# Performance work log

Measured on AMD Instinct MI355X. Metric: run time of the kernel, lower is better.

## Reference

```python
import jax, jax.numpy as jnp
import numpy as np

D_MODEL = 512
STATE_DIM = 6
D_STATE = 16
D_CONV = 4
EXPAND = 2
D_INNER = EXPAND * D_MODEL            # 1024
DT_RANK = -(-D_MODEL // 16)           # ceil(d_model/16) = 32


def setup_inputs() -> dict:
    key = jax.random.key(0)
    ks = jax.random.split(key, 12)
    s = 0.02
    return {
        "features": jax.random.normal(ks[0], (32, 2048, D_MODEL), dtype=jnp.float32),
        # Mamba params (mamba_ssm defaults: in/out_proj bias=False, conv+dt_proj bias=True)
        "in_proj_w": jax.random.normal(ks[1], (2 * D_INNER, D_MODEL), dtype=jnp.float32) * s,
        "conv_w": jax.random.normal(ks[2], (D_INNER, D_CONV), dtype=jnp.float32) * s,
        "conv_b": jnp.zeros((D_INNER,), dtype=jnp.float32),
        "x_proj_w": jax.random.normal(ks[3], (DT_RANK + 2 * D_STATE, D_INNER), dtype=jnp.float32) * s,
        "dt_proj_w": jax.random.normal(ks[4], (D_INNER, DT_RANK), dtype=jnp.float32) * s,
        "dt_proj_b": jax.random.normal(ks[5], (D_INNER,), dtype=jnp.float32) * s,
        "A_log": jnp.log(jnp.broadcast_to(jnp.arange(1, D_STATE + 1, dtype=jnp.float32), (D_INNER, D_STATE))),
        "D": jnp.ones((D_INNER,), dtype=jnp.float32),
        "out_proj_w": jax.random.normal(ks[6], (D_MODEL, D_INNER), dtype=jnp.float32) * s,
        # trailing fc head: d_model -> state_dim**2
        "fc_w": jax.random.normal(ks[7], (STATE_DIM * STATE_DIM, D_MODEL), dtype=jnp.float32) * s,
        "fc_b": jnp.zeros((STATE_DIM * STATE_DIM,), dtype=jnp.float32),
    }


def reference(features, in_proj_w, conv_w, conv_b, x_proj_w, dt_proj_w, dt_proj_b,
              A_log, D, out_proj_w, fc_w, fc_b):
    # Original loops Mamba over timesteps with seq_len=1 slices -> each timestep is
    # independent. Flatten (batch, seq) into one token axis and vectorize.
    B_, T, dm = features.shape
    f = features.reshape(B_ * T, dm)                      # (N, d_model)

    xz = f @ in_proj_w.T                                  # (N, 2*d_inner)
    x, z = jnp.split(xz, 2, axis=-1)
    # causal depthwise conv on a length-1 sequence: only the last tap contributes
    x = jax.nn.silu(x * conv_w[:, -1] + conv_b)           # (N, d_inner)

    x_dbl = x @ x_proj_w.T                                # (N, dt_rank + 2*d_state)
    dt = x_dbl[:, :DT_RANK]
    Bm = x_dbl[:, DT_RANK:DT_RANK + D_STATE]              # (N, d_state)
    Cm = x_dbl[:, DT_RANK + D_STATE:]                     # (N, d_state)
    delta = jax.nn.softplus(dt @ dt_proj_w.T + dt_proj_b) # (N, d_inner)

    # single-step selective scan with h0 = 0:
    #   h = exp(delta*A)*0 + delta*B*x ;  y = sum_s C_s h_s + D*x
    # (A_log therefore never affects the output for seq_len=1 calls)
    bc = jnp.sum(Bm * Cm, axis=-1, keepdims=True)         # (N, 1)
    y = delta * x * bc + D * x                            # (N, d_inner)
    y = y * jax.nn.silu(z)

    out = y @ out_proj_w.T                                # (N, d_model)
    A_flat = out @ fc_w.T + fc_b                          # (N, state_dim**2)
    return A_flat.reshape(B_, T, STATE_DIM, STATE_DIM)
```

## Files before the change

kernel.cpp:

```cpp
#include <hip/hip_runtime.h>

typedef unsigned short u16;
typedef unsigned int u32;
typedef __attribute__((ext_vector_type(8))) short bf16x8;
typedef __attribute__((ext_vector_type(4))) float f32x4;

#define NTOK 65536
#define DM 512
#define DI 1024

__device__ __forceinline__ float bf2f(u16 u){ u32 x=((u32)u)<<16; float f; __builtin_memcpy(&f,&x,4); return f; }
__device__ __forceinline__ u16 f2bf(float f){ u32 u; __builtin_memcpy(&u,&f,4); u += 0x7fffu + ((u>>16)&1u); return (u16)(u>>16); }
__device__ __forceinline__ float siluf(float x){ return x/(1.f+__expf(-x)); }
__device__ __forceinline__ float softplus_fast(float x){
  float l = __logf(1.f + __expf(x));
  return (x > 20.f) ? x : l;
}

__device__ __forceinline__ void gload_lds16(const void* g, void* l){
  __builtin_amdgcn_global_load_lds((const __attribute__((address_space(1))) u32*)g,
                                   (__attribute__((address_space(3))) u32*)l, 16, 0, 0);
}

__global__ void k_sentinel(float* out){ out[0] = 1.2345e6f; }

__global__ void k_cast_bf16(const float* __restrict__ in, u16* __restrict__ out, int n){
  int i = (blockIdx.x*256 + threadIdx.x)*4;
  if (i >= n) return;
  float4 v = *(const float4*)(in + i);
  ushort4 o; o.x=f2bf(v.x); o.y=f2bf(v.y); o.z=f2bf(v.z); o.w=f2bf(v.w);
  *(ushort4*)(out + i) = o;
}

__global__ void k_make_wa(const float* __restrict__ fcw, const float* __restrict__ opw,
                          u16* __restrict__ wa){
  int j = blockIdx.x*256 + threadIdx.x;
  int i = blockIdx.y;
  float s = 0.f;
  if (i < 36){
    const float* fr = fcw + i*DM;
    #pragma unroll 8
    for (int k=0;k<DM;++k) s += fr[k]*opw[(size_t)k*DI + j];
  }
  wa[(size_t)i*DI + j] = f2bf(s);
}

__global__ __launch_bounds__(256) void k_gemm_xz(
  const u16* __restrict__ A, const u16* __restrict__ B,
  const float* __restrict__ convw, const float* __restrict__ convb,
  u16* __restrict__ xp, u16* __restrict__ zs)
{
  __shared__ u16 smem[32768];
  u16* SA = smem;
  u16* SB = smem + 16384;
  const int tid=threadIdx.x, wv=tid>>6, ln=tid&63;
  const int l15=ln&15, l4=ln>>4, h=l15&7;
  const int c0g=blockIdx.x*128, r0=blockIdx.y*128;
  const int wm=wv>>1, wn=wv&1;
  const int sr=ln>>3, scs=((ln&7)^sr)*8;
  const int chk0=(l4^h)*8, chk1=((l4+4)^h)*8;
  const int rA=(wm*64+l15)*64, rB=(wn*64+l15)*64;
  f32x4 acc[4][4]={};

  auto STAGE=[&](int buf, int k0){
    u16* Ad = SA + buf*8192;
    u16* Bd = SB + buf*8192;
    #pragma unroll
    for (int it=0;it<4;++it){
      int c=wv*4+it;
      gload_lds16(A + (size_t)(r0 + c*8 + sr)*DM + k0 + scs, Ad + c*512);
    }
    #pragma unroll
    for (int it=0;it<4;++it){
      int c=wv*4+it;
      gload_lds16(B + (size_t)(c0g + c*8 + sr)*DM + k0 + scs, Bd + c*512);
    }
  };

  STAGE(0, 0);
  __syncthreads();
  __builtin_amdgcn_sched_barrier(0);
  int cur = 0;
  #pragma clang loop unroll(disable)
  for (int t=0;t<8;++t){
    if (t < 7) STAGE(cur^1, (t+1)*64);
    const u16* Ac = SA + cur*8192;
    const u16* Bc = SB + cur*8192;
    #pragma unroll
    for (int kk=0;kk<2;++kk){
      const int ch = kk ? chk1 : chk0;
      bf16x8 af[4], bfr[4];
      #pragma unroll
      for (int m=0;m<4;++m) af[m]=*(const bf16x8*)(Ac + rA + m*1024 + ch);
      #pragma unroll
      for (int n=0;n<4;++n) bfr[n]=*(const bf16x8*)(Bc + rB + n*1024 + ch);
      #pragma unroll
      for (int m=0;m<4;++m)
        #pragma unroll
        for (int n=0;n<4;++n)
          acc[m][n]=__builtin_amdgcn_mfma_f32_16x16x32_bf16(af[m],bfr[n],acc[m][n],0,0,0);
    }
    __syncthreads();
    __builtin_amdgcn_sched_barrier(0);
    cur ^= 1;
  }

  const bool isx = (c0g < DI);
  const int cc0 = isx ? c0g : c0g - DI;
  u16* ep = smem;
  #pragma unroll
  for (int n=0;n<4;++n){
    int tcol = wn*64 + n*16 + l15;
    int gcol = c0g + tcol;
    float cw = isx ? convw[gcol*4+3] : 0.f;
    float cb = isx ? convb[gcol]     : 0.f;
    #pragma unroll
    for (int m=0;m<4;++m){
      int trow = wm*64 + m*16 + l4*4;
      #pragma unroll
      for (int r=0;r<4;++r){
        float v = acc[m][n][r];
        float o = isx ? siluf(v*cw + cb) : siluf(v);
        ep[(trow+r)*160 + tcol] = f2bf(o);
      }
    }
  }
  __syncthreads();
  int rrow = tid>>1, half = tid&1;
  const u16* srcp = ep + rrow*160 + half*64;
  u16* dst = (isx ? xp : zs) + (size_t)(r0+rrow)*DI + cc0 + half*64;
  #pragma unroll
  for (int j=0;j<8;++j)
    *(int4*)(dst + j*8) = *(const int4*)(srcp + j*8);
}

__global__ void k_bcdt(const float* __restrict__ xd, u16* __restrict__ dtb, float* __restrict__ bc){
  int t = blockIdx.x*256 + threadIdx.x;
  if (t >= NTOK) return;
  const float4* p = (const float4*)(xd + (size_t)t*64);
  #pragma unroll
  for (int q=0;q<8;++q){
    float4 v = p[q];
    ushort4 o; o.x=f2bf(v.x); o.y=f2bf(v.y); o.z=f2bf(v.z); o.w=f2bf(v.w);
    *(ushort4*)(dtb + (size_t)t*32 + q*4) = o;
  }
  float s=0.f;
  #pragma unroll
  for (int q=0;q<4;++q){
    float4 b = p[8+q], c = p[12+q];
    s += b.x*c.x + b.y*c.y + b.z*c.z + b.w*c.w;
  }
  bc[t]=s;
}

template<int EPI>
__global__ __launch_bounds__(256) void k_gemm_n64(
  const u16* __restrict__ A, const u16* __restrict__ B,
  float* __restrict__ xd, const float* __restrict__ fcb, float* __restrict__ out)
{
  __shared__ u16 smem[24576];
  u16* SA = smem;
  u16* SB = smem + 16384;
  const int tid=threadIdx.x, wv=tid>>6, ln=tid&63;
  const int l15=ln&15, l4=ln>>4, h=l15&7;
  const int r0=blockIdx.x*128;
  const int wm=wv>>1, wn=wv&1;
  const int sr=ln>>3, scs=((ln&7)^sr)*8;
  const int chk0=(l4^h)*8, chk1=((l4+4)^h)*8;
  const int rA=(wm*64+l15)*64, rB=(wn*32+l15)*64;
  f32x4 acc[4][2]={};

  auto STAGE=[&](int buf, int k0){
    u16* Ad = SA + buf*8192;
    u16* Bd = SB + buf*4096;
    #pragma unroll
    for (int it=0;it<4;++it){
      int c=wv*4+it;
      gload_lds16(A + (size_t)(r0 + c*8 + sr)*DI + k0 + scs, Ad + c*512);
    }
    #pragma unroll
    for (int it=0;it<2;++it){
      int c=wv*2+it;
      gload_lds16(B + (size_t)(c*8 + sr)*DI + k0 + scs, Bd + c*512);
    }
  };

  STAGE(0, 0);
  __syncthreads();
  __builtin_amdgcn_sched_barrier(0);
  int cur = 0;
  #pragma clang loop unroll(disable)
  for (int t=0;t<16;++t){
    if (t < 15) STAGE(cur^1, (t+1)*64);
    const u16* Ac = SA + cur*8192;
    const u16* Bc = SB + cur*4096;
    #pragma unroll
    for (int kk=0;kk<2;++kk){
      const int ch = kk ? chk1 : chk0;
      bf16x8 af[4], bfr[2];
      #pragma unroll
      for (int m=0;m<4;++m) af[m]=*(const bf16x8*)(Ac + rA + m*1024 + ch);
      #pragma unroll
      for (int n=0;n<2;++n) bfr[n]=*(const bf16x8*)(Bc + rB + n*1024 + ch);
      #pragma unroll
      for (int m=0;m<4;++m)
        #pragma unroll
        for (int n=0;n<2;++n)
          acc[m][n]=__builtin_amdgcn_mfma_f32_16x16x32_bf16(af[m],bfr[n],acc[m][n],0,0,0);
    }
    __syncthreads();
    __builtin_amdgcn_sched_barrier(0);
    cur ^= 1;
  }
  #pragma unroll
  for (int n=0;n<2;++n){
    int j = wn*32 + n*16 + l15;
    #pragma unroll
    for (int m=0;m<4;++m){
      #pragma unroll
      for (int r=0;r<4;++r){
        int t = r0 + wm*64 + m*16 + l4*4 + r;
        float v = acc[m][n][r];
        if (EPI==0) xd[(size_t)t*64 + j] = v;
        else if (j < 36) out[(size_t)t*36 + j] = v + fcb[j];
      }
    }
  }
}

__global__ __launch_bounds__(256) void k_delta_y(
  const u16* __restrict__ dtb, const u16* __restrict__ Bw,
  const float* __restrict__ dpb, const float* __restrict__ Dv,
  const float* __restrict__ bc,
  const u16* __restrict__ xp, u16* __restrict__ zy)
{
  __shared__ u16 smem[17408];
  u16* As = smem;
  u16* Bs = smem + 4096;
  const int tid=threadIdx.x, wv=tid>>6, ln=tid&63;
  const int l15=ln&15, l4=ln>>4;
  const int c0=blockIdx.x*128, r0=blockIdx.y*128;
  const int wm=wv>>1, wn=wv&1;
  const int sr=ln>>2, sc=(ln&3)*8;
  #pragma unroll
  for (int it=0;it<2;++it){
    int c=wv*2+it;
    gload_lds16(dtb + (size_t)(r0 + c*16 + sr)*32 + sc, As + c*512);
  }
  #pragma unroll
  for (int it=0;it<2;++it){
    int c=wv*2+it;
    gload_lds16(Bw + (size_t)(c0 + c*16 + sr)*32 + sc, Bs + c*512);
  }
  __syncthreads();
  __builtin_amdgcn_sched_barrier(0);
  f32x4 acc[4][4]={};
  bf16x8 af[4], bfr[4];
  #pragma unroll
  for (int m=0;m<4;++m) af[m]=*(const bf16x8*)(As + (wm*64+m*16+l15)*32 + l4*8);
  #pragma unroll
  for (int n=0;n<4;++n) bfr[n]=*(const bf16x8*)(Bs + (wn*64+n*16+l15)*32 + l4*8);
  #pragma unroll
  for (int m=0;m<4;++m)
    #pragma unroll
    for (int n=0;n<4;++n)
      acc[m][n]=__builtin_amdgcn_mfma_f32_16x16x32_bf16(af[m],bfr[n],acc[m][n],0,0,0);
  __syncthreads();
  u16* W = smem;
  #pragma unroll
  for (int n=0;n<4;++n){
    int tcol = wn*64 + n*16 + l15;
    int j = c0 + tcol;
    float dpbj = dpb[j], Dj = Dv[j];
    #pragma unroll
    for (int m=0;m<4;++m){
      int trow = wm*64 + m*16 + l4*4;
      #pragma unroll
      for (int r=0;r<4;++r){
        float delta = softplus_fast(acc[m][n][r] + dpbj);
        float w = delta*bc[r0 + trow + r] + Dj;
        W[(trow+r)*136 + tcol] = f2bf(w);
      }
    }
  }
  __syncthreads();
  const int row = tid>>1, half = tid&1;
  const u16* wp = W + row*136 + half*64;
  const size_t gbase = (size_t)(r0 + row)*DI + c0 + half*64;
  const u16* xpp = xp + gbase;
  u16* zp = zy + gbase;
  #pragma unroll
  for (int q=0;q<8;++q){
    bf16x8 wv8 = *(const bf16x8*)(wp + q*8);
    bf16x8 xv  = *(const bf16x8*)(xpp + q*8);
    bf16x8 zv  = *(const bf16x8*)(zp + q*8);
    bf16x8 ov;
    #pragma unroll
    for (int e=0;e<8;++e){
      float y = bf2f((u16)wv8[e]) * bf2f((u16)xv[e]) * bf2f((u16)zv[e]);
      ov[e] = (short)f2bf(y);
    }
    *(bf16x8*)(zp + q*8) = ov;
  }
}

extern "C" void kernel_launch(void* const* d_in, const int* in_sizes, int n_in,
                              void* d_out, int out_size, void* d_ws, size_t ws_size,
                              hipStream_t stream){
  const float* f      = (const float*)d_in[0];
  const float* inpw   = (const float*)d_in[1];
  const float* convw  = (const float*)d_in[2];
  const float* convb  = (const float*)d_in[3];
  const float* xprojw = (const float*)d_in[4];
  const float* dtpw   = (const float*)d_in[5];
  const float* dtpb   = (const float*)d_in[6];
  const float* Dv     = (const float*)d_in[8];
  const float* opw    = (const float*)d_in[9];
  const float* fcw    = (const float*)d_in[10];
  const float* fcb    = (const float*)d_in[11];
  float* out = (float*)d_out;

  char* ws = (char*)d_ws;
  size_t off = 0;
  auto alloc = [&](size_t sz)->void*{ void* p = ws + off; off += (sz + 255) & ~(size_t)255; return p; };
  u16*   fbf = (u16*)  alloc((size_t)NTOK*DM*2);
  u16*   xp  = (u16*)  alloc((size_t)NTOK*DI*2);
  u16*   zy  = (u16*)  alloc((size_t)NTOK*DI*2);
  float* xd  = (float*)alloc((size_t)NTOK*64*4);
  u16*   dtb = (u16*)  alloc((size_t)NTOK*32*2);
  float* bc  = (float*)alloc((size_t)NTOK*4);
  u16*   ipw = (u16*)  alloc((size_t)2048*512*2);
  u16*   xpw = (u16*)  alloc((size_t)64*1024*2);
  u16*   dpw = (u16*)  alloc((size_t)1024*32*2);
  u16*   wa  = (u16*)  alloc((size_t)64*1024*2);
  if (off > ws_size){ k_sentinel<<<1,1,0,stream>>>(out); return; }

  k_cast_bf16<<<dim3((NTOK*DM/4)/256),256,0,stream>>>(f, fbf, NTOK*DM);
  k_cast_bf16<<<dim3((2048*512/4)/256),256,0,stream>>>(inpw, ipw, 2048*512);
  k_cast_bf16<<<dim3((64*1024/4)/256),256,0,stream>>>(xprojw, xpw, 64*1024);
  k_cast_bf16<<<dim3((1024*32/4)/256),256,0,stream>>>(dtpw, dpw, 1024*32);
  k_make_wa<<<dim3(4,64),256,0,stream>>>(fcw, opw, wa);

  k_gemm_xz<<<dim3(16,512),256,0,stream>>>(fbf, ipw, convw, convb, xp, zy);
  k_gemm_n64<0><<<dim3(512),256,0,stream>>>(xp, xpw, xd, nullptr, nullptr);
  k_bcdt<<<dim3(NTOK/256),256,0,stream>>>(xd, dtb, bc);
  k_delta_y<<<dim3(8,512),256,0,stream>>>(dtb, dpw, dtpb, Dv, bc, xp, zy);
  k_gemm_n64<1><<<dim3(512),256,0,stream>>>(zy, wa, nullptr, fcb, out);
}
```

Measured before the change: 539.3 us.

## Triple-buffer xz GEMM with 8 waves, XCD-aware tile order, fuse bcdt into x_proj epilogue

The in_proj GEMM now runs 512-thread blocks, with each wave computing a 32x64 sub-tile. It uses a three-stage LDS ring with explicit vmcnt waits and a single barrier per k-step, and remaps the 1D grid so that blocks sharing a row tile land on the same XCD for L2 reuse. The k_bcdt kernel and its fp32 xd intermediate are removed. The x_proj GEMM epilogue now writes bf16 dt and the B·C dot product directly through LDS. This cuts one launch and a 16MB round trip, at the cost of larger LDS use and lower occupancy in the main GEMM.

```diff
diff --git a/kernel.cpp b/kernel.cpp
--- a/kernel.cpp
+++ b/kernel.cpp
@@ -45,65 +45,67 @@
   wa[(size_t)i*DI + j] = f2bf(s);
 }
 
-__global__ __launch_bounds__(256) void k_gemm_xz(
+__global__ __launch_bounds__(512) void k_gemm_xz(
   const u16* __restrict__ A, const u16* __restrict__ B,
   const float* __restrict__ convw, const float* __restrict__ convb,
   u16* __restrict__ xp, u16* __restrict__ zs)
 {
-  __shared__ u16 smem[32768];
-  u16* SA = smem;
-  u16* SB = smem + 16384;
+  __shared__ u16 smem[49152];
   const int tid=threadIdx.x, wv=tid>>6, ln=tid&63;
   const int l15=ln&15, l4=ln>>4, h=l15&7;
-  const int c0g=blockIdx.x*128, r0=blockIdx.y*128;
+  const int d = blockIdx.x;
+  const int xcd = d & 7, q = d >> 3;
+  const int g = xcd + 8*(q >> 4);
+  const int mcb = q & 15;
+  const int r0 = g*128, c0g = mcb*128;
   const int wm=wv>>1, wn=wv&1;
   const int sr=ln>>3, scs=((ln&7)^sr)*8;
   const int chk0=(l4^h)*8, chk1=((l4+4)^h)*8;
-  const int rA=(wm*64+l15)*64, rB=(wn*64+l15)*64;
-  f32x4 acc[4][4]={};
-
-  auto STAGE=[&](int buf, int k0){
-    u16* Ad = SA + buf*8192;
-    u16* Bd = SB + buf*8192;
-    #pragma unroll
-    for (int it=0;it<4;++it){
-      int c=wv*4+it;
+  f32x4 acc[2][4]={};
+
+  auto STAGE=[&](int buf, int kt){
+    const int k0 = kt*64;
+    u16* Ad = smem + buf*16384;
+    u16* Bd = Ad + 8192;
+    #pragma unroll
+    for (int it=0;it<2;++it){
+      int c=wv*2+it;
       gload_lds16(A + (size_t)(r0 + c*8 + sr)*DM + k0 + scs, Ad + c*512);
     }
     #pragma unroll
-    for (int it=0;it<4;++it){
-      int c=wv*4+it;
+    for (int it=0;it<2;++it){
+      int c=wv*2+it;
       gload_lds16(B + (size_t)(c0g + c*8 + sr)*DM + k0 + scs, Bd + c*512);
     }
   };
 
-  STAGE(0, 0);
-  __syncthreads();
-  __builtin_amdgcn_sched_barrier(0);
-  int cur = 0;
+  STAGE(0,0); STAGE(1,1);
   #pragma clang loop unroll(disable)
   for (int t=0;t<8;++t){
-    if (t < 7) STAGE(cur^1, (t+1)*64);
-    const u16* Ac = SA + cur*8192;
-    const u16* Bc = SB + cur*8192;
+    if (t<7) asm volatile("s_waitcnt vmcnt(4)" ::: "memory");
+    else     asm volatile("s_waitcnt vmcnt(0)" ::: "memory");
+    __builtin_amdgcn_s_barrier();
+    __builtin_amdgcn_sched_barrier(0);
+    if (t+2<8) STAGE((t+2)%3, t+2);
+    const u16* Ac = smem + (t%3)*16384;
+    const u16* Bc = Ac + 8192;
     #pragma unroll
     for (int kk=0;kk<2;++kk){
       const int ch = kk ? chk1 : chk0;
-      bf16x8 af[4], bfr[4];
-      #pragma unroll
-      for (int m=0;m<4;++m) af[m]=*(const bf16x8*)(Ac + rA + m*1024 + ch);
-      #pragma unroll
-      for (int n=0;n<4;++n) bfr[n]=*(const bf16x8*)(Bc + rB + n*1024 + ch);
-      #pragma unroll
-      for (int m=0;m<4;++m)
+      bf16x8 af[2], bfr[4];
+      #pragma unroll
+      for (int m=0;m<2;++m) af[m]=*(const bf16x8*)(Ac + (wm*32+m*16+l15)*64 + ch);
+      #pragma unroll
+      for (int n=0;n<4;++n) bfr[n]=*(const bf16x8*)(Bc + (wn*64+n*16+l15)*64 + ch);
+      #pragma unroll
+      for (int m=0;m<2;++m)
         #pragma unroll
         for (int n=0;n<4;++n)
           acc[m][n]=__builtin_amdgcn_mfma_f32_16x16x32_bf16(af[m],bfr[n],acc[m][n],0,0,0);
     }
-    __syncthreads();
     __builtin_amdgcn_sched_barrier(0);
-    cur ^= 1;
-  }
+  }
+  __syncthreads();
 
   const bool isx = (c0g < DI);
   const int cc0 = isx ? c0g : c0g - DI;
@@ -115,8 +117,8 @@
     float cw = isx ? convw[gcol*4+3] : 0.f;
     float cb = isx ? convb[gcol]     : 0.f;
     #pragma unroll
-    for (int m=0;m<4;++m){
-      int trow = wm*64 + m*16 + l4*4;
+    for (int m=0;m<2;++m){
+      int trow = wm*32 + m*16 + l4*4;
       #pragma unroll
       for (int r=0;r<4;++r){
         float v = acc[m][n][r];
@@ -126,37 +128,19 @@
     }
   }
   __syncthreads();
-  int rrow = tid>>1, half = tid&1;
-  const u16* srcp = ep + rrow*160 + half*64;
-  u16* dst = (isx ? xp : zs) + (size_t)(r0+rrow)*DI + cc0 + half*64;
-  #pragma unroll
-  for (int j=0;j<8;++j)
-    *(int4*)(dst + j*8) = *(const int4*)(srcp + j*8);
-}
-
-__global__ void k_bcdt(const float* __restrict__ xd, u16* __restrict__ dtb, float* __restrict__ bc){
-  int t = blockIdx.x*256 + threadIdx.x;
-  if (t >= NTOK) return;
-  const float4* p = (const float4*)(xd + (size_t)t*64);
-  #pragma unroll
-  for (int q=0;q<8;++q){
-    float4 v = p[q];
-    ushort4 o; o.x=f2bf(v.x); o.y=f2bf(v.y); o.z=f2bf(v.z); o.w=f2bf(v.w);
-    *(ushort4*)(dtb + (size_t)t*32 + q*4) = o;
-  }
-  float s=0.f;
-  #pragma unroll
-  for (int q=0;q<4;++q){
-    float4 b = p[8+q], c = p[12+q];
-    s += b.x*c.x + b.y*c.y + b.z*c.z + b.w*c.w;
-  }
-  bc[t]=s;
+  const int rrow = tid>>2, qq = tid&3;
+  const u16* srcp = ep + rrow*160 + qq*32;
+  u16* dst = (isx ? xp : zs) + (size_t)(r0+rrow)*DI + cc0 + qq*32;
+  #pragma unroll
+  for (int j=0;j<4;++j)
+    ((int4*)dst)[j] = ((const int4*)srcp)[j];
 }
 
 template<int EPI>
 __global__ __launch_bounds__(256) void k_gemm_n64(
   const u16* __restrict__ A, const u16* __restrict__ B,
-  float* __restrict__ xd, const float* __restrict__ fcb, float* __restrict__ out)
+  u16* __restrict__ dtb, float* __restrict__ bc,
+  const float* __restrict__ fcb, float* __restrict__ out)
 {
   __shared__ u16 smem[24576];
   u16* SA = smem;
@@ -212,17 +196,49 @@
     __builtin_amdgcn_sched_barrier(0);
     cur ^= 1;
   }
-  #pragma unroll
-  for (int n=0;n<2;++n){
-    int j = wn*32 + n*16 + l15;
-    #pragma unroll
-    for (int m=0;m<4;++m){
-      #pragma unroll
-      for (int r=0;r<4;++r){
-        int t = r0 + wm*64 + m*16 + l4*4 + r;
-        float v = acc[m][n][r];
-        if (EPI==0) xd[(size_t)t*64 + j] = v;
-        else if (j < 36) out[(size_t)t*36 + j] = v + fcb[j];
+
+  if (EPI==0){
+    float* W = (float*)smem;
+    #pragma unroll
+    for (int n=0;n<2;++n){
+      int j = wn*32 + n*16 + l15;
+      #pragma unroll
+      for (int m=0;m<4;++m){
+        int trow = wm*64 + m*16 + l4*4;
+        #pragma unroll
+        for (int r=0;r<4;++r)
+          W[(trow+r)*68 + j] = acc[m][n][r];
+      }
+    }
+    __syncthreads();
+    const int row = tid>>1, half = tid&1;
+    const float* wr = W + row*68;
+    if (half==0){
+      u16* dst = dtb + (size_t)(r0+row)*32;
+      #pragma unroll
+      for (int qv=0;qv<4;++qv){
+        bf16x8 o;
+        #pragma unroll
+        for (int e=0;e<8;++e) o[e] = (short)f2bf(wr[qv*8+e]);
+        *(bf16x8*)(dst + qv*8) = o;
+      }
+    } else {
+      float s=0.f;
+      #pragma unroll
+      for (int e=0;e<16;++e) s += wr[32+e]*wr[48+e];
+      bc[r0+row] = s;
+    }
+  } else {
+    #pragma unroll
+    for (int n=0;n<2;++n){
+      int j = wn*32 + n*16 + l15;
+      #pragma unroll
+      for (int m=0;m<4;++m){
+        #pragma unroll
+        for (int r=0;r<4;++r){
+          int t = r0 + wm*64 + m*16 + l4*4 + r;
+          if (j < 36) out[(size_t)t*36 + j] = acc[m][n][r] + fcb[j];
+        }
       }
     }
   }
@@ -326,7 +342,6 @@
   u16*   fbf = (u16*)  alloc((size_t)NTOK*DM*2);
   u16*   xp  = (u16*)  alloc((size_t)NTOK*DI*2);
   u16*   zy  = (u16*)  alloc((size_t)NTOK*DI*2);
-  float* xd  = (float*)alloc((size_t)NTOK*64*4);
   u16*   dtb = (u16*)  alloc((size_t)NTOK*32*2);
   float* bc  = (float*)alloc((size_t)NTOK*4);
   u16*   ipw = (u16*)  alloc((size_t)2048*512*2);
@@ -341,9 +356,8 @@
   k_cast_bf16<<<dim3((1024*32/4)/256),256,0,stream>>>(dtpw, dpw, 1024*32);
   k_make_wa<<<dim3(4,64),256,0,stream>>>(fcw, opw, wa);
 
-  k_gemm_xz<<<dim3(16,512),256,0,stream>>>(fbf, ipw, convw, convb, xp, zy);
-  k_gemm_n64<0><<<dim3(512),256,0,stream>>>(xp, xpw, xd, nullptr, nullptr);
-  k_bcdt<<<dim3(NTOK/256),256,0,stream>>>(xd, dtb, bc);
+  k_gemm_xz<<<dim3(8192),512,0,stream>>>(fbf, ipw, convw, convb, xp, zy);
+  k_gemm_n64<0><<<dim3(512),256,0,stream>>>(xp, xpw, dtb, bc, nullptr, nullptr);
   k_delta_y<<<dim3(8,512),256,0,stream>>>(dtb, dpw, dtpb, Dv, bc, xp, zy);
-  k_gemm_n64<1><<<dim3(512),256,0,stream>>>(zy, wa, nullptr, fcb, out);
-}
+  k_gemm_n64<1><<<dim3(512),256,0,stream>>>(zy, wa, nullptr, nullptr, fcb, out);
+}
```

New measurement: 583.5 us. +8.2%, slower.

## Fuse delta/y gating with folded output GEMM and bc/dt epilogue into x_proj

Applied to the files above, without the earlier changes.

Moves the dt cast and B·C dot product into the x_proj GEMM epilogue through an LDS staging tile, so the separate bcdt kernel and the fp32 xd buffer go away. It also merges the delta/y elementwise kernel with the final out_proj·fc GEMM. Each block now loops over all 1024 inner channels in 128-wide chunks, keeps y in LDS, and accumulates the 64-wide output directly, so the y tensor is never written back and re-read from global memory. In exchange the grid drops from 4096 blocks to 512, LDS use per block rises, and the wa weights are read straight from global memory without LDS staging, which may lower occupancy and overlap.

```diff
diff --git a/kernel.cpp b/kernel.cpp
--- a/kernel.cpp
+++ b/kernel.cpp
@@ -134,29 +134,9 @@
     *(int4*)(dst + j*8) = *(const int4*)(srcp + j*8);
 }
 
-__global__ void k_bcdt(const float* __restrict__ xd, u16* __restrict__ dtb, float* __restrict__ bc){
-  int t = blockIdx.x*256 + threadIdx.x;
-  if (t >= NTOK) return;
-  const float4* p = (const float4*)(xd + (size_t)t*64);
-  #pragma unroll
-  for (int q=0;q<8;++q){
-    float4 v = p[q];
-    ushort4 o; o.x=f2bf(v.x); o.y=f2bf(v.y); o.z=f2bf(v.z); o.w=f2bf(v.w);
-    *(ushort4*)(dtb + (size_t)t*32 + q*4) = o;
-  }
-  float s=0.f;
-  #pragma unroll
-  for (int q=0;q<4;++q){
-    float4 b = p[8+q], c = p[12+q];
-    s += b.x*c.x + b.y*c.y + b.z*c.z + b.w*c.w;
-  }
-  bc[t]=s;
-}
-
-template<int EPI>
 __global__ __launch_bounds__(256) void k_gemm_n64(
   const u16* __restrict__ A, const u16* __restrict__ B,
-  float* __restrict__ xd, const float* __restrict__ fcb, float* __restrict__ out)
+  u16* __restrict__ dtb, float* __restrict__ bc)
 {
   __shared__ u16 smem[24576];
   u16* SA = smem;
@@ -212,36 +192,56 @@
     __builtin_amdgcn_sched_barrier(0);
     cur ^= 1;
   }
+
+  float* W = (float*)smem;
   #pragma unroll
   for (int n=0;n<2;++n){
     int j = wn*32 + n*16 + l15;
     #pragma unroll
     for (int m=0;m<4;++m){
-      #pragma unroll
-      for (int r=0;r<4;++r){
-        int t = r0 + wm*64 + m*16 + l4*4 + r;
-        float v = acc[m][n][r];
-        if (EPI==0) xd[(size_t)t*64 + j] = v;
-        else if (j < 36) out[(size_t)t*36 + j] = v + fcb[j];
-      }
-    }
-  }
-}
-
-__global__ __launch_bounds__(256) void k_delta_y(
+      int trow = wm*64 + m*16 + l4*4;
+      #pragma unroll
+      for (int r=0;r<4;++r)
+        W[(trow+r)*68 + j] = acc[m][n][r];
+    }
+  }
+  __syncthreads();
+  const int row = tid>>1, half = tid&1;
+  const float* wr = W + row*68;
+  if (half==0){
+    u16* dst = dtb + (size_t)(r0+row)*32;
+    #pragma unroll
+    for (int qv=0;qv<4;++qv){
+      bf16x8 o;
+      #pragma unroll
+      for (int e=0;e<8;++e) o[e] = (short)f2bf(wr[qv*8+e]);
+      *(bf16x8*)(dst + qv*8) = o;
+    }
+  } else {
+    float s=0.f;
+    #pragma unroll
+    for (int e=0;e<16;++e) s += wr[32+e]*wr[48+e];
+    bc[r0+row] = s;
+  }
+}
+
+__global__ __launch_bounds__(256) void k_fused(
   const u16* __restrict__ dtb, const u16* __restrict__ Bw,
   const float* __restrict__ dpb, const float* __restrict__ Dv,
   const float* __restrict__ bc,
-  const u16* __restrict__ xp, u16* __restrict__ zy)
+  const u16* __restrict__ xp, const u16* __restrict__ zs,
+  const u16* __restrict__ wa,
+  const float* __restrict__ fcb, float* __restrict__ out)
 {
-  __shared__ u16 smem[17408];
-  u16* As = smem;
-  u16* Bs = smem + 4096;
+  __shared__ u16 As[4096];
+  __shared__ u16 Bs[2][4096];
+  __shared__ u16 Y[128*136];
   const int tid=threadIdx.x, wv=tid>>6, ln=tid&63;
   const int l15=ln&15, l4=ln>>4;
-  const int c0=blockIdx.x*128, r0=blockIdx.y*128;
+  const int r0=blockIdx.x*128;
   const int wm=wv>>1, wn=wv&1;
   const int sr=ln>>2, sc=(ln&3)*8;
+
   #pragma unroll
   for (int it=0;it<2;++it){
     int c=wv*2+it;
@@ -250,57 +250,108 @@
   #pragma unroll
   for (int it=0;it<2;++it){
     int c=wv*2+it;
-    gload_lds16(Bw + (size_t)(c0 + c*16 + sr)*32 + sc, Bs + c*512);
+    gload_lds16(Bw + (size_t)(c*16 + sr)*32 + sc, Bs[0] + c*512);
   }
   __syncthreads();
   __builtin_amdgcn_sched_barrier(0);
-  f32x4 acc[4][4]={};
-  bf16x8 af[4], bfr[4];
+
+  bf16x8 af[4];
   #pragma unroll
   for (int m=0;m<4;++m) af[m]=*(const bf16x8*)(As + (wm*64+m*16+l15)*32 + l4*8);
-  #pragma unroll
-  for (int n=0;n<4;++n) bfr[n]=*(const bf16x8*)(Bs + (wn*64+n*16+l15)*32 + l4*8);
-  #pragma unroll
-  for (int m=0;m<4;++m)
-    #pragma unroll
-    for (int n=0;n<4;++n)
-      acc[m][n]=__builtin_amdgcn_mfma_f32_16x16x32_bf16(af[m],bfr[n],acc[m][n],0,0,0);
-  __syncthreads();
-  u16* W = smem;
+
+  f32x4 oacc[2][4]={};
+  const int yrow = tid>>1, yhalf = tid&1;
+  int cur = 0;
+
+  #pragma clang loop unroll(disable)
+  for (int ch=0; ch<8; ++ch){
+    f32x4 dacc[4][4]={};
+    bf16x8 bfr[4];
+    #pragma unroll
+    for (int n=0;n<4;++n) bfr[n]=*(const bf16x8*)(Bs[cur] + (wn*64+n*16+l15)*32 + l4*8);
+    #pragma unroll
+    for (int m=0;m<4;++m)
+      #pragma unroll
+      for (int n=0;n<4;++n)
+        dacc[m][n]=__builtin_amdgcn_mfma_f32_16x16x32_bf16(af[m],bfr[n],dacc[m][n],0,0,0);
+    if (ch<7){
+      #pragma unroll
+      for (int it=0;it<2;++it){
+        int c=wv*2+it;
+        gload_lds16(Bw + (size_t)((ch+1)*128 + c*16 + sr)*32 + sc, Bs[cur^1] + c*512);
+      }
+    }
+    #pragma unroll
+    for (int n=0;n<4;++n){
+      int tcol = wn*64 + n*16 + l15;
+      int j = ch*128 + tcol;
+      float dpbj = dpb[j], Dj = Dv[j];
+      #pragma unroll
+      for (int m=0;m<4;++m){
+        int trow = wm*64 + m*16 + l4*4;
+        #pragma unroll
+        for (int r=0;r<4;++r){
+          float delta = softplus_fast(dacc[m][n][r] + dpbj);
+          float w = delta*bc[r0 + trow + r] + Dj;
+          Y[(trow+r)*136 + tcol] = f2bf(w);
+        }
+      }
+    }
+    __syncthreads();
+    {
+      u16* wp = Y + yrow*136 + yhalf*64;
+      const size_t gbase = (size_t)(r0 + yrow)*DI + ch*128 + yhalf*64;
+      const u16* xpp = xp + gbase;
+      const u16* zp  = zs + gbase;
+      #pragma unroll
+      for (int q=0;q<8;++q){
+        bf16x8 wv8 = *(const bf16x8*)(wp + q*8);
+        bf16x8 xv  = *(const bf16x8*)(xpp + q*8);
+        bf16x8 zv  = *(const bf16x8*)(zp + q*8);
+        bf16x8 ov;
+        #pragma unroll
+        for (int e=0;e<8;++e){
+          float y = bf2f((u16)wv8[e]) * bf2f((u16)xv[e]) * bf2f((u16)zv[e]);
+          ov[e] = (short)f2bf(y);
+        }
+        *(bf16x8*)(wp + q*8) = ov;
+      }
+    }
+    __syncthreads();
+    #pragma unroll
+    for (int kk=0;kk<4;++kk){
+      bf16x8 af2[2], bf2r[4];
+      #pragma unroll
+      for (int m=0;m<2;++m)
+        af2[m]=*(const bf16x8*)(Y + (wv*32 + m*16 + l15)*136 + kk*32 + l4*8);
+      #pragma unroll
+      for (int n=0;n<4;++n)
+        bf2r[n]=*(const bf16x8*)(wa + (size_t)(n*16 + l15)*DI + ch*128 + kk*32 + l4*8);
+      #pragma unroll
+      for (int m=0;m<2;++m)
+        #pragma unroll
+        for (int n=0;n<4;++n)
+          oacc[m][n]=__builtin_amdgcn_mfma_f32_16x16x32_bf16(af2[m],bf2r[n],oacc[m][n],0,0,0);
+    }
+    __syncthreads();
+    __builtin_amdgcn_sched_barrier(0);
+    cur ^= 1;
+  }
+
   #pragma unroll
   for (int n=0;n<4;++n){
-    int tcol = wn*64 + n*16 + l15;
-    int j = c0 + tcol;
-    float dpbj = dpb[j], Dj = Dv[j];
-    #pragma unroll
-    for (int m=0;m<4;++m){
-      int trow = wm*64 + m*16 + l4*4;
-      #pragma unroll
-      for (int r=0;r<4;++r){
-        float delta = softplus_fast(acc[m][n][r] + dpbj);
-        float w = delta*bc[r0 + trow + r] + Dj;
-        W[(trow+r)*136 + tcol] = f2bf(w);
-      }
-    }
-  }
-  __syncthreads();
-  const int row = tid>>1, half = tid&1;
-  const u16* wp = W + row*136 + half*64;
-  const size_t gbase = (size_t)(r0 + row)*DI + c0 + half*64;
-  const u16* xpp = xp + gbase;
-  u16* zp = zy + gbase;
-  #pragma unroll
-  for (int q=0;q<8;++q){
-    bf16x8 wv8 = *(const bf16x8*)(wp + q*8);
-    bf16x8 xv  = *(const bf16x8*)(xpp + q*8);
-    bf16x8 zv  = *(const bf16x8*)(zp + q*8);
-    bf16x8 ov;
-    #pragma unroll
-    for (int e=0;e<8;++e){
-      float y = bf2f((u16)wv8[e]) * bf2f((u16)xv[e]) * bf2f((u16)zv[e]);
-      ov[e] = (short)f2bf(y);
-    }
-    *(bf16x8*)(zp + q*8) = ov;
+    int j = n*16 + l15;
+    if (j < 36){
+      float fj = fcb[j];
+      #pragma unroll
+      for (int m=0;m<2;++m){
+        #pragma unroll
+        for (int r=0;r<4;++r){
+          int t = r0 + wv*32 + m*16 + l4*4 + r;
+          out[(size_t)t*36 + j] = oacc[m][n][r] + fj;
+        }
+      }
+    }
   }
 }
 
@@ -326,7 +377,6 @@
   u16*   fbf = (u16*)  alloc((size_t)NTOK*DM*2);
   u16*   xp  = (u16*)  alloc((size_t)NTOK*DI*2);
   u16*   zy  = (u16*)  alloc((size_t)NTOK*DI*2);
-  float* xd  = (float*)alloc((size_t)NTOK*64*4);
   u16*   dtb = (u16*)  alloc((size_t)NTOK*32*2);
   float* bc  = (float*)alloc((size_t)NTOK*4);
   u16*   ipw = (u16*)  alloc((size_t)2048*512*2);
@@ -342,8 +392,6 @@
   k_make_wa<<<dim3(4,64),256,0,stream>>>(fcw, opw, wa);
 
   k_gemm_xz<<<dim3(16,512),256,0,stream>>>(fbf, ipw, convw, convb, xp, zy);
-  k_gemm_n64<0><<<dim3(512),256,0,stream>>>(xp, xpw, xd, nullptr, nullptr);
-  k_bcdt<<<dim3(NTOK/256),256,0,stream>>>(xd, dtb, bc);
-  k_delta_y<<<dim3(8,512),256,0,stream>>>(dtb, dpw, dtpb, Dv, bc, xp, zy);
-  k_gemm_n64<1><<<dim3(512),256,0,stream>>>(zy, wa, nullptr, fcb, out);
-}
+  k_gemm_n64<<<dim3(512),256,0,stream>>>(xp, xpw, dtb, bc);
+  k_fused<<<dim3(512),256,0,stream>>>(dtb, dpw, dtpb, Dv, bc, xp, zy, wa, fcb, out);
+}
```

Result: faster. 501.5 us (-7.0%).
